# Kernel optimization log

Hardware: AMD Instinct MI355X
Metric: run time of the kernel (lower is better)

## Reference

```python
import jax, jax.numpy as jnp
import numpy as np

HIDDEN = 4096
N_EXPERTS = 128
TOP_K = 8
N_GROUP = 8
TOPK_GROUP = 4
ROUTED_SCALE = 1.0
NORM_TOPK = True
T = 32768


def setup_inputs() -> dict:
    key = jax.random.key(0)
    k1, k2, k3 = jax.random.split(key, 3)
    hidden_states = jax.random.normal(k1, (T, HIDDEN), dtype=jnp.float32)
    weight = jax.random.normal(k2, (N_EXPERTS, HIDDEN), dtype=jnp.float32) * 0.02
    e_score_correction_bias = jax.random.normal(k3, (N_EXPERTS,), dtype=jnp.float32) * 0.1
    return {"hidden_states": hidden_states, "weight": weight,
            "e_score_correction_bias": e_score_correction_bias}


def reference(hidden_states, weight, e_score_correction_bias):
    # GLM4-MoE top-k router: linear -> sigmoid -> bias-corrected grouped top-k
    x = hidden_states.reshape(-1, HIDDEN)
    router_logits = jnp.einsum('th,eh->te', x, weight)          # [T, E]
    scores = jax.nn.sigmoid(router_logits)                      # [T, E]
    scores_for_choice = scores + e_score_correction_bias[None, :]

    per_group = N_EXPERTS // N_GROUP
    g = scores_for_choice.reshape(-1, N_GROUP, per_group)       # [T, G, E/G]
    # group score = sum of top-2 expert scores within each group
    group_scores = jax.lax.top_k(g, 2)[0].sum(axis=-1)          # [T, G]
    group_idx = jax.lax.top_k(group_scores, TOPK_GROUP)[1]      # [T, topk_group]
    group_mask = jax.nn.one_hot(group_idx, N_GROUP, dtype=scores.dtype).sum(axis=1)  # [T, G]
    score_mask = jnp.repeat(group_mask, per_group, axis=-1)     # [T, E]
    masked_scores = jnp.where(score_mask > 0, scores_for_choice, 0.0)

    topk_indices = jax.lax.top_k(masked_scores, TOP_K)[1]       # [T, top_k]
    topk_weights = jnp.take_along_axis(scores, topk_indices, axis=1)  # gather raw (un-biased) scores
    if NORM_TOPK:
        denom = topk_weights.sum(axis=-1, keepdims=True) + 1e-20
        topk_weights = topk_weights / denom
    topk_weights = topk_weights * ROUTED_SCALE
    return topk_indices, topk_weights
```

## Files before the change

kernel.cpp:

```cpp
#include <hip/hip_runtime.h>
#include <math.h>

#define T_TOKENS 32768
#define HIDDEN   4096
#define NEXP     128
#define TM       64
#define BK       32
#define NSTAGE   (HIDDEN / BK)

#define A_PLANE_EL    2048
#define A_BUF_EL      (2 * A_PLANE_EL)
#define B_BASE_EL     (2 * A_BUF_EL)
#define B_PLANE_EL    4096
#define B_BUF_EL      (2 * B_PLANE_EL)
#define LDS_ELEMS     (B_BASE_EL + 2 * B_BUF_EL)
#define B_BASE_BYTES  (B_BASE_EL * 2)
#define B_BUF_BYTES   (B_BUF_EL * 2)
#define SC_STRIDE     129
#define B_CHUNK_BYTES B_BUF_BYTES
#define WS_BYTES ((size_t)NSTAGE * B_CHUNK_BYTES)

typedef _Float16 f16x8 __attribute__((ext_vector_type(8)));
typedef float f32x4  __attribute__((ext_vector_type(4)));

__device__ __forceinline__ void split2(float x, _Float16& h0, _Float16& h1) {
    _Float16 a = (_Float16)x;
    float af = (float)a;
    if (__builtin_fabsf(af) < 6.103515625e-05f) { a = (_Float16)0.0f; af = 0.0f; }
    h0 = a;
    h1 = (_Float16)((x - af) * 4096.0f);
}

__global__ __launch_bounds__(256) void presplit_w(
    const float* __restrict__ w, _Float16* __restrict__ ws16)
{
    const int g = blockIdx.x * 256 + threadIdx.x;
    const int l = g & 63;
    const int t = (g >> 6) & 7;
    const int s = g >> 9;
    const int e  = t * 16 + (l & 15);
    const int kb = s * BK + ((l >> 4) & 3) * 8;
    const float* src = w + (size_t)e * HIDDEN + kb;
    float4 v0 = *(const float4*)(src);
    float4 v1 = *(const float4*)(src + 4);
    float vv[8] = {v0.x, v0.y, v0.z, v0.w, v1.x, v1.y, v1.z, v1.w};
    _Float16 h0[8], h1[8];
#pragma unroll
    for (int j = 0; j < 8; ++j) split2(vv[j], h0[j], h1[j]);
    _Float16* dst = ws16 + (size_t)s * 8192 + (t * 64 + l) * 8;
    *(f16x8*)(dst)        = (f16x8){h0[0],h0[1],h0[2],h0[3],h0[4],h0[5],h0[6],h0[7]};
    *(f16x8*)(dst + 4096) = (f16x8){h1[0],h1[1],h1[2],h1[3],h1[4],h1[5],h1[6],h1[7]};
}

__global__ __launch_bounds__(256, 2) void glm4_router_mfma(
    const float* __restrict__ x, const _Float16* __restrict__ wsplit,
    const float* __restrict__ bias, float* __restrict__ out)
{
    __shared__ __align__(16) _Float16 lds[LDS_ELEMS];

    const int tid  = threadIdx.x;
    const int wid  = tid >> 6;
    const int lane = tid & 63;
    const int rt_base = (wid & 1) * 2;
    const int ct_base = (wid >> 1) * 4;
    const int tok_base = blockIdx.x * TM;

    const int arow = (tid >> 6) * 16 + (tid & 15);
    const int akoff = ((tid >> 4) & 3) * 8;
    const float* xsrc = x + (size_t)(tok_base + arow) * HIDDEN + akoff;
    const int awr = tid * 8;

    f32x4 mainA[2][4];
    f32x4 corr[2][4];
    double accd[2][4][4];
#pragma unroll
    for (int r = 0; r < 2; ++r)
#pragma unroll
        for (int c = 0; c < 4; ++c) {
            mainA[r][c] = (f32x4){0.f, 0.f, 0.f, 0.f};
            corr[r][c]  = (f32x4){0.f, 0.f, 0.f, 0.f};
#pragma unroll
            for (int v = 0; v < 4; ++v) accd[r][c][v] = 0.0;
        }

#define GLDS_B(S, BUF) do {                                                    \
    const char* gsrc_ = (const char*)wsplit + (size_t)(S) * B_CHUNK_BYTES + tid * 16; \
    char* ldst_ = (char*)lds + B_BASE_BYTES + (BUF) * B_BUF_BYTES + tid * 16;  \
    __builtin_amdgcn_global_load_lds(                                          \
        (const __attribute__((address_space(1))) unsigned*)(gsrc_),            \
        (__attribute__((address_space(3))) unsigned*)(ldst_), 16, 0, 0);       \
    __builtin_amdgcn_global_load_lds(                                          \
        (const __attribute__((address_space(1))) unsigned*)(gsrc_ + 4096),     \
        (__attribute__((address_space(3))) unsigned*)(ldst_ + 4096), 16, 0, 0);\
    __builtin_amdgcn_global_load_lds(                                          \
        (const __attribute__((address_space(1))) unsigned*)(gsrc_ + 8192),     \
        (__attribute__((address_space(3))) unsigned*)(ldst_ + 8192), 16, 0, 0);\
    __builtin_amdgcn_global_load_lds(                                          \
        (const __attribute__((address_space(1))) unsigned*)(gsrc_ + 12288),    \
        (__attribute__((address_space(3))) unsigned*)(ldst_ + 12288), 16, 0, 0);\
} while (0)

#define SPLIT_A(XV0, XV1, BUF) do {                                            \
    float vv_[8] = {(XV0).x, (XV0).y, (XV0).z, (XV0).w,                        \
                    (XV1).x, (XV1).y, (XV1).z, (XV1).w};                       \
    _Float16 h0_[8], h1_[8];                                                   \
    _Pragma("unroll")                                                          \
    for (int j = 0; j < 8; ++j) split2(vv_[j], h0_[j], h1_[j]);                \
    _Float16* ab_ = &lds[(BUF) * A_BUF_EL + awr];                              \
    *(f16x8*)(ab_) = (f16x8){h0_[0],h0_[1],h0_[2],h0_[3],                      \
                             h0_[4],h0_[5],h0_[6],h0_[7]};                     \
    *(f16x8*)(ab_ + A_PLANE_EL) = (f16x8){h1_[0],h1_[1],h1_[2],h1_[3],         \
                                          h1_[4],h1_[5],h1_[6],h1_[7]};        \
} while (0)

#define MFMA_COL(C, B0_, B1_) do {                                             \
    _Pragma("unroll")                                                          \
    for (int r = 0; r < 2; ++r) {                                              \
        mainA[r][C] = __builtin_amdgcn_mfma_f32_16x16x32_f16(Af0[r], B0_, mainA[r][C], 0, 0, 0); \
        corr[r][C]  = __builtin_amdgcn_mfma_f32_16x16x32_f16(Af0[r], B1_, corr[r][C], 0, 0, 0);  \
        corr[r][C]  = __builtin_amdgcn_mfma_f32_16x16x32_f16(Af1[r], B0_, corr[r][C], 0, 0, 0);  \
    }                                                                          \
} while (0)

#define BCOL(C, BUF, B0_, B1_)                                                 \
    f16x8 B0_ = *(const f16x8*)(&lds[B_BASE_EL + (BUF) * B_BUF_EL              \
                      + ((ct_base + (C)) * 64 + lane) * 8]);                   \
    f16x8 B1_ = *(const f16x8*)(&lds[B_BASE_EL + (BUF) * B_BUF_EL              \
                      + B_PLANE_EL + ((ct_base + (C)) * 64 + lane) * 8]);

#define BODY(S, BUF, XC0, XC1, XL0, XL1) do {                                  \
    GLDS_B((S) + 1, (BUF) ^ 1);                                                \
    {                                                                          \
        int s2_ = (S) + 2; if (s2_ > NSTAGE - 1) s2_ = NSTAGE - 1;             \
        XL0 = *(const float4*)(xsrc + (size_t)s2_ * BK);                       \
        XL1 = *(const float4*)(xsrc + (size_t)s2_ * BK + 4);                   \
    }                                                                          \
    f16x8 Af0[2], Af1[2];                                                      \
    _Pragma("unroll")                                                          \
    for (int r = 0; r < 2; ++r) {                                              \
        Af0[r] = *(const f16x8*)(&lds[(BUF) * A_BUF_EL                         \
                                      + ((rt_base + r) * 64 + lane) * 8]);     \
        Af1[r] = *(const f16x8*)(&lds[(BUF) * A_BUF_EL + A_PLANE_EL            \
                                      + ((rt_base + r) * 64 + lane) * 8]);     \
    }                                                                          \
    {                                                                          \
        BCOL(0, BUF, Bc00, Bc01);                                              \
        BCOL(1, BUF, Bc10, Bc11);                                              \
        __builtin_amdgcn_s_setprio(1);                                         \
        MFMA_COL(0, Bc00, Bc01);                                               \
        MFMA_COL(1, Bc10, Bc11);                                               \
        __builtin_amdgcn_s_setprio(0);                                         \
    }                                                                          \
    SPLIT_A(XC0, XC1, (BUF) ^ 1);   \
    {                                                                          \
        BCOL(2, BUF, Bc20, Bc21);                                              \
        BCOL(3, BUF, Bc30, Bc31);                                              \
        __builtin_amdgcn_s_setprio(1);                                         \
        MFMA_COL(2, Bc20, Bc21);                                               \
        MFMA_COL(3, Bc30, Bc31);                                               \
        __builtin_amdgcn_s_setprio(0);                                         \
    }                                                                          \
    if (((S) & 3) == 3) {                                                      \
        _Pragma("unroll")                                                      \
        for (int r = 0; r < 2; ++r)                                            \
            _Pragma("unroll")                                                  \
            for (int c = 0; c < 4; ++c) {                                      \
                _Pragma("unroll")                                              \
                for (int v = 0; v < 4; ++v)                                    \
                    accd[r][c][v] += (double)mainA[r][c][v]                    \
                                   + (double)corr[r][c][v] * (1.0 / 4096.0);   \
                mainA[r][c] = (f32x4){0.f, 0.f, 0.f, 0.f};                     \
                corr[r][c]  = (f32x4){0.f, 0.f, 0.f, 0.f};                     \
            }                                                                  \
    }                                                                          \
    __syncthreads();       \
} while (0)

    float4 xA0, xA1, xB0, xB1;
    {
        float4 x00 = *(const float4*)(xsrc);
        float4 x01 = *(const float4*)(xsrc + 4);
        GLDS_B(0, 0);
        xA0 = *(const float4*)(xsrc + BK);
        xA1 = *(const float4*)(xsrc + BK + 4);
        SPLIT_A(x00, x01, 0);
    }
    __syncthreads();

    for (int s = 0; s < NSTAGE - 2; s += 2) {
        BODY(s, 0, xA0, xA1, xB0, xB1);
        BODY(s + 1, 1, xB0, xB1, xA0, xA1);
    }
    BODY(NSTAGE - 2, 0, xA0, xA1, xB0, xB1);

    {
        f16x8 Af0[2], Af1[2];
#pragma unroll
        for (int r = 0; r < 2; ++r) {
            Af0[r] = *(const f16x8*)(&lds[1 * A_BUF_EL
                                          + ((rt_base + r) * 64 + lane) * 8]);
            Af1[r] = *(const f16x8*)(&lds[1 * A_BUF_EL + A_PLANE_EL
                                          + ((rt_base + r) * 64 + lane) * 8]);
        }
#pragma unroll
        for (int c = 0; c < 4; ++c) {
            f16x8 B0_ = *(const f16x8*)(&lds[B_BASE_EL + 1 * B_BUF_EL
                              + ((ct_base + c) * 64 + lane) * 8]);
            f16x8 B1_ = *(const f16x8*)(&lds[B_BASE_EL + 1 * B_BUF_EL
                              + B_PLANE_EL + ((ct_base + c) * 64 + lane) * 8]);
#pragma unroll
            for (int r = 0; r < 2; ++r) {
                mainA[r][c] = __builtin_amdgcn_mfma_f32_16x16x32_f16(Af0[r], B0_, mainA[r][c], 0, 0, 0);
                corr[r][c]  = __builtin_amdgcn_mfma_f32_16x16x32_f16(Af0[r], B1_, corr[r][c], 0, 0, 0);
                corr[r][c]  = __builtin_amdgcn_mfma_f32_16x16x32_f16(Af1[r], B0_, corr[r][c], 0, 0, 0);
            }
        }
#pragma unroll
        for (int r = 0; r < 2; ++r)
#pragma unroll
            for (int c = 0; c < 4; ++c)
#pragma unroll
                for (int v = 0; v < 4; ++v)
                    accd[r][c][v] += (double)mainA[r][c][v]
                                   + (double)corr[r][c][v] * (1.0 / 4096.0);
    }

    __syncthreads();
    float* sc = (float*)lds;
#pragma unroll
    for (int r = 0; r < 2; ++r)
#pragma unroll
        for (int c = 0; c < 4; ++c) {
#pragma unroll
            for (int v = 0; v < 4; ++v) {
                const int tokl = (rt_base + r) * 16 + (lane >> 4) * 4 + v;
                const int e    = (ct_base + c) * 16 + (lane & 15);
                const float lg = (float)accd[r][c][v];
                const float sg = (float)(1.0 / (1.0 + exp(-(double)lg)));
                sc[tokl * SC_STRIDE + e] = sg + bias[e];
            }
        }
    __syncthreads();

    if (tid < TM) {
        const float* scp = sc + tid * SC_STRIDE;

        float gsc[8];
#pragma unroll
        for (int g = 0; g < 8; ++g) {
            float m1 = -1e30f, m2 = -1e30f;
#pragma unroll
            for (int j = 0; j < 16; ++j) {
                const float v = scp[g * 16 + j];
                if (v > m1) { m2 = m1; m1 = v; }
                else if (v > m2) { m2 = v; }
            }
            gsc[g] = m1 + m2;
        }

        unsigned gmask = 0;
#pragma unroll
        for (int p = 0; p < 4; ++p) {
            float best = -1e30f; int bi = 0;
#pragma unroll
            for (int g = 0; g < 8; ++g) {
                const bool taken = (gmask >> g) & 1u;
                if (!taken && gsc[g] > best) { best = gsc[g]; bi = g; }
            }
            gmask |= 1u << bi;
        }

        unsigned long long chosen0 = 0ull, chosen1 = 0ull;
        int   idxs[8];
        float wts[8];
#pragma unroll
        for (int p = 0; p < 8; ++p) {
            float best = -1e30f; int bi = 0;
            for (int e = 0; e < NEXP; ++e) {
                const bool sel = (gmask >> (e >> 4)) & 1u;
                const float v = sel ? scp[e] : 0.0f;
                const bool ch = (e < 64) ? ((chosen0 >> e) & 1ull)
                                         : ((chosen1 >> (e - 64)) & 1ull);
                if (!ch && v > best) { best = v; bi = e; }
            }
            if (bi < 64) chosen0 |= 1ull << bi; else chosen1 |= 1ull << (bi - 64);
            idxs[p] = bi;
            wts[p] = scp[bi] - bias[bi];
        }

        float denom = 0.0f;
#pragma unroll
        for (int p = 0; p < 8; ++p) denom += wts[p];
        denom += 1e-20f;

        const size_t row = (size_t)(tok_base + tid) * 8;
        float* outI = out;
        float* outW = out + (size_t)T_TOKENS * 8;
#pragma unroll
        for (int p = 0; p < 8; ++p) {
            outI[row + p] = (float)idxs[p];
            outW[row + p] = wts[p] / denom;
        }
    }
}

extern "C" void kernel_launch(void* const* d_in, const int* in_sizes, int n_in,
                              void* d_out, int out_size, void* d_ws, size_t ws_size,
                              hipStream_t stream) {
    const float* x    = (const float*)d_in[0];
    const float* w    = (const float*)d_in[1];
    const float* bias = (const float*)d_in[2];
    float* out = (float*)d_out;
    _Float16* ws16 = (_Float16*)d_ws;

    presplit_w<<<dim3(NSTAGE * 8 * 64 / 256), 256, 0, stream>>>(w, ws16);
    glm4_router_mfma<<<dim3(T_TOKENS / TM), 256, 0, stream>>>(x, ws16, bias, out);
}
```

Measured before the change: 239.2 us.

## Keep split A fragments in registers instead of staging through LDS

Measured after the change: 256.8 us. 7.4% more time.

```diff
diff --git a/kernel.cpp b/kernel.cpp
--- a/kernel.cpp
+++ b/kernel.cpp
@@ -8,14 +8,10 @@
 #define BK       32
 #define NSTAGE   (HIDDEN / BK)
 
-#define A_PLANE_EL    2048
-#define A_BUF_EL      (2 * A_PLANE_EL)
-#define B_BASE_EL     (2 * A_BUF_EL)
 #define B_PLANE_EL    4096
 #define B_BUF_EL      (2 * B_PLANE_EL)
-#define LDS_ELEMS     (B_BASE_EL + 2 * B_BUF_EL)
-#define B_BASE_BYTES  (B_BASE_EL * 2)
 #define B_BUF_BYTES   (B_BUF_EL * 2)
+#define LDS_ELEMS     16512
 #define SC_STRIDE     129
 #define B_CHUNK_BYTES B_BUF_BYTES
 #define WS_BYTES ((size_t)NSTAGE * B_CHUNK_BYTES)
@@ -65,10 +61,11 @@
     const int ct_base = (wid >> 1) * 4;
     const int tok_base = blockIdx.x * TM;
 
-    const int arow = (tid >> 6) * 16 + (tid & 15);
-    const int akoff = ((tid >> 4) & 3) * 8;
-    const float* xsrc = x + (size_t)(tok_base + arow) * HIDDEN + akoff;
-    const int awr = tid * 8;
+    const int lrow  = lane & 15;
+    const int lkoct = (lane >> 4) & 3;
+    const float* xr0 = x + (size_t)(tok_base + (wid & 1) * 32 + lrow) * HIDDEN
+                         + lkoct * 8;
+    const float* xr1 = xr0 + (size_t)16 * HIDDEN;
 
     f32x4 mainA[2][4];
     f32x4 corr[2][4];
@@ -85,7 +82,7 @@
 
 #define GLDS_B(S, BUF) do {                                                    \
     const char* gsrc_ = (const char*)wsplit + (size_t)(S) * B_CHUNK_BYTES + tid * 16; \
-    char* ldst_ = (char*)lds + B_BASE_BYTES + (BUF) * B_BUF_BYTES + tid * 16;  \
+    char* ldst_ = (char*)lds + (BUF) * B_BUF_BYTES + tid * 16;                 \
     __builtin_amdgcn_global_load_lds(                                          \
         (const __attribute__((address_space(1))) unsigned*)(gsrc_),            \
         (__attribute__((address_space(3))) unsigned*)(ldst_), 16, 0, 0);       \
@@ -100,64 +97,56 @@
         (__attribute__((address_space(3))) unsigned*)(ldst_ + 12288), 16, 0, 0);\
 } while (0)
 
-#define SPLIT_A(XV0, XV1, BUF) do {                                            \
+#define SPLIT_REG(XV0, XV1, OUT0, OUT1) do {                                   \
     float vv_[8] = {(XV0).x, (XV0).y, (XV0).z, (XV0).w,                        \
                     (XV1).x, (XV1).y, (XV1).z, (XV1).w};                       \
     _Float16 h0_[8], h1_[8];                                                   \
     _Pragma("unroll")                                                          \
     for (int j = 0; j < 8; ++j) split2(vv_[j], h0_[j], h1_[j]);                \
-    _Float16* ab_ = &lds[(BUF) * A_BUF_EL + awr];                              \
-    *(f16x8*)(ab_) = (f16x8){h0_[0],h0_[1],h0_[2],h0_[3],                      \
-                             h0_[4],h0_[5],h0_[6],h0_[7]};                     \
-    *(f16x8*)(ab_ + A_PLANE_EL) = (f16x8){h1_[0],h1_[1],h1_[2],h1_[3],         \
-                                          h1_[4],h1_[5],h1_[6],h1_[7]};        \
+    OUT0 = (f16x8){h0_[0],h0_[1],h0_[2],h0_[3],h0_[4],h0_[5],h0_[6],h0_[7]};   \
+    OUT1 = (f16x8){h1_[0],h1_[1],h1_[2],h1_[3],h1_[4],h1_[5],h1_[6],h1_[7]};   \
 } while (0)
 
-#define MFMA_COL(C, B0_, B1_) do {                                             \
+#define MFMA_COL(C, B0_, B1_, CA0, CA1) do {                                   \
     _Pragma("unroll")                                                          \
     for (int r = 0; r < 2; ++r) {                                              \
-        mainA[r][C] = __builtin_amdgcn_mfma_f32_16x16x32_f16(Af0[r], B0_, mainA[r][C], 0, 0, 0); \
-        corr[r][C]  = __builtin_amdgcn_mfma_f32_16x16x32_f16(Af0[r], B1_, corr[r][C], 0, 0, 0);  \
-        corr[r][C]  = __builtin_amdgcn_mfma_f32_16x16x32_f16(Af1[r], B0_, corr[r][C], 0, 0, 0);  \
+        mainA[r][C] = __builtin_amdgcn_mfma_f32_16x16x32_f16(CA0[r], B0_, mainA[r][C], 0, 0, 0); \
+        corr[r][C]  = __builtin_amdgcn_mfma_f32_16x16x32_f16(CA0[r], B1_, corr[r][C], 0, 0, 0);  \
+        corr[r][C]  = __builtin_amdgcn_mfma_f32_16x16x32_f16(CA1[r], B0_, corr[r][C], 0, 0, 0);  \
     }                                                                          \
 } while (0)
 
 #define BCOL(C, BUF, B0_, B1_)                                                 \
-    f16x8 B0_ = *(const f16x8*)(&lds[B_BASE_EL + (BUF) * B_BUF_EL              \
+    f16x8 B0_ = *(const f16x8*)(&lds[(BUF) * B_BUF_EL                          \
                       + ((ct_base + (C)) * 64 + lane) * 8]);                   \
-    f16x8 B1_ = *(const f16x8*)(&lds[B_BASE_EL + (BUF) * B_BUF_EL              \
-                      + B_PLANE_EL + ((ct_base + (C)) * 64 + lane) * 8]);
-
-#define BODY(S, BUF, XC0, XC1, XL0, XL1) do {                                  \
+    f16x8 B1_ = *(const f16x8*)(&lds[(BUF) * B_BUF_EL + B_PLANE_EL             \
+                      + ((ct_base + (C)) * 64 + lane) * 8]);
+
+#define BODY(S, BUF, CA0, CA1, NA0, NA1, XC0, XC1, XC2, XC3, XL0, XL1, XL2, XL3) do { \
     GLDS_B((S) + 1, (BUF) ^ 1);                                                \
     {                                                                          \
         int s2_ = (S) + 2; if (s2_ > NSTAGE - 1) s2_ = NSTAGE - 1;             \
-        XL0 = *(const float4*)(xsrc + (size_t)s2_ * BK);                       \
-        XL1 = *(const float4*)(xsrc + (size_t)s2_ * BK + 4);                   \
-    }                                                                          \
-    f16x8 Af0[2], Af1[2];                                                      \
-    _Pragma("unroll")                                                          \
-    for (int r = 0; r < 2; ++r) {                                              \
-        Af0[r] = *(const f16x8*)(&lds[(BUF) * A_BUF_EL                         \
-                                      + ((rt_base + r) * 64 + lane) * 8]);     \
-        Af1[r] = *(const f16x8*)(&lds[(BUF) * A_BUF_EL + A_PLANE_EL            \
-                                      + ((rt_base + r) * 64 + lane) * 8]);     \
+        XL0 = *(const float4*)(xr0 + (size_t)s2_ * BK);                        \
+        XL1 = *(const float4*)(xr0 + (size_t)s2_ * BK + 4);                    \
+        XL2 = *(const float4*)(xr1 + (size_t)s2_ * BK);                        \
+        XL3 = *(const float4*)(xr1 + (size_t)s2_ * BK + 4);                    \
     }                                                                          \
     {                                                                          \
         BCOL(0, BUF, Bc00, Bc01);                                              \
         BCOL(1, BUF, Bc10, Bc11);                                              \
         __builtin_amdgcn_s_setprio(1);                                         \
-        MFMA_COL(0, Bc00, Bc01);                                               \
-        MFMA_COL(1, Bc10, Bc11);                                               \
+        MFMA_COL(0, Bc00, Bc01, CA0, CA1);                                     \
+        MFMA_COL(1, Bc10, Bc11, CA0, CA1);                                     \
         __builtin_amdgcn_s_setprio(0);                                         \
     }                                                                          \
-    SPLIT_A(XC0, XC1, (BUF) ^ 1);   \
+    SPLIT_REG(XC0, XC1, NA0[0], NA1[0]);       \
+    SPLIT_REG(XC2, XC3, NA0[1], NA1[1]);                                       \
     {                                                                          \
         BCOL(2, BUF, Bc20, Bc21);                                              \
         BCOL(3, BUF, Bc30, Bc31);                                              \
         __builtin_amdgcn_s_setprio(1);                                         \
-        MFMA_COL(2, Bc20, Bc21);                                               \
-        MFMA_COL(3, Bc30, Bc31);                                               \
+        MFMA_COL(2, Bc20, Bc21, CA0, CA1);                                     \
+        MFMA_COL(3, Bc30, Bc31, CA0, CA1);                                     \
         __builtin_amdgcn_s_setprio(0);                                         \
     }                                                                          \
     if (((S) & 3) == 3) {                                                      \
@@ -176,43 +165,39 @@
     __syncthreads();       \
 } while (0)
 
-    float4 xA0, xA1, xB0, xB1;
+    f16x8 Aa0[2], Aa1[2], Ab0[2], Ab1[2];
+    float4 xA0, xA1, xA2, xA3, xB0, xB1, xB2, xB3;
+
     {
-        float4 x00 = *(const float4*)(xsrc);
-        float4 x01 = *(const float4*)(xsrc + 4);
+        float4 c0 = *(const float4*)(xr0);
+        float4 c1 = *(const float4*)(xr0 + 4);
+        float4 c2 = *(const float4*)(xr1);
+        float4 c3 = *(const float4*)(xr1 + 4);
         GLDS_B(0, 0);
-        xA0 = *(const float4*)(xsrc + BK);
-        xA1 = *(const float4*)(xsrc + BK + 4);
-        SPLIT_A(x00, x01, 0);
+        xA0 = *(const float4*)(xr0 + BK);
+        xA1 = *(const float4*)(xr0 + BK + 4);
+        xA2 = *(const float4*)(xr1 + BK);
+        xA3 = *(const float4*)(xr1 + BK + 4);
+        SPLIT_REG(c0, c1, Aa0[0], Aa1[0]);
+        SPLIT_REG(c2, c3, Aa0[1], Aa1[1]);
     }
     __syncthreads();
 
     for (int s = 0; s < NSTAGE - 2; s += 2) {
-        BODY(s, 0, xA0, xA1, xB0, xB1);
-        BODY(s + 1, 1, xB0, xB1, xA0, xA1);
+        BODY(s, 0, Aa0, Aa1, Ab0, Ab1, xA0, xA1, xA2, xA3, xB0, xB1, xB2, xB3);
+        BODY(s + 1, 1, Ab0, Ab1, Aa0, Aa1, xB0, xB1, xB2, xB3, xA0, xA1, xA2, xA3);
     }
-    BODY(NSTAGE - 2, 0, xA0, xA1, xB0, xB1);
+    BODY(NSTAGE - 2, 0, Aa0, Aa1, Ab0, Ab1, xA0, xA1, xA2, xA3, xB0, xB1, xB2, xB3);
 
     {
-        f16x8 Af0[2], Af1[2];
-#pragma unroll
-        for (int r = 0; r < 2; ++r) {
-            Af0[r] = *(const f16x8*)(&lds[1 * A_BUF_EL
-                                          + ((rt_base + r) * 64 + lane) * 8]);
-            Af1[r] = *(const f16x8*)(&lds[1 * A_BUF_EL + A_PLANE_EL
-                                          + ((rt_base + r) * 64 + lane) * 8]);
-        }
 #pragma unroll
         for (int c = 0; c < 4; ++c) {
-            f16x8 B0_ = *(const f16x8*)(&lds[B_BASE_EL + 1 * B_BUF_EL
-                              + ((ct_base + c) * 64 + lane) * 8]);
-            f16x8 B1_ = *(const f16x8*)(&lds[B_BASE_EL + 1 * B_BUF_EL
-                              + B_PLANE_EL + ((ct_base + c) * 64 + lane) * 8]);
+            BCOL(c, 1, B0_, B1_);
 #pragma unroll
             for (int r = 0; r < 2; ++r) {
-                mainA[r][c] = __builtin_amdgcn_mfma_f32_16x16x32_f16(Af0[r], B0_, mainA[r][c], 0, 0, 0);
-                corr[r][c]  = __builtin_amdgcn_mfma_f32_16x16x32_f16(Af0[r], B1_, corr[r][c], 0, 0, 0);
-                corr[r][c]  = __builtin_amdgcn_mfma_f32_16x16x32_f16(Af1[r], B0_, corr[r][c], 0, 0, 0);
+                mainA[r][c] = __builtin_amdgcn_mfma_f32_16x16x32_f16(Ab0[r], B0_, mainA[r][c], 0, 0, 0);
+                corr[r][c]  = __builtin_amdgcn_mfma_f32_16x16x32_f16(Ab0[r], B1_, corr[r][c], 0, 0, 0);
+                corr[r][c]  = __builtin_amdgcn_mfma_f32_16x16x32_f16(Ab1[r], B0_, corr[r][c], 0, 0, 0);
             }
         }
 #pragma unroll
```
